# Kernel tuning notes

Measured on AMD Instinct MI355X. Metric: run time of the kernel, lower is better.

Reference implementation:

```python
import jax, jax.numpy as jnp
import numpy as np
import math

NUM_HEADS = 16
CONSTITUENCY_PENALTY = 0.5
CONSTITUENT_BLOCK = 64  # deterministic stand-in for the ChomskyParser constituency spans


def constituency_penalty_mask(seq_len, dtype):
    # Tokens in the same constituent (contiguous block) attend freely;
    # cross-constituent pairs are penalized by CONSTITUENCY_PENALTY.
    blk = jnp.arange(seq_len) // CONSTITUENT_BLOCK
    return jnp.where(blk[:, None] != blk[None, :], CONSTITUENCY_PENALTY, 0.0).astype(dtype)


def setup_inputs() -> dict:
    key = jax.random.key(0)
    ks = jax.random.split(key, 7)
    B, S, H = 8, 1024, 1024
    scale = 1.0 / math.sqrt(H)
    return {
        "hidden_states": jax.random.normal(ks[0], (B, S, H), jnp.float32),
        "Wq": jax.random.normal(ks[1], (H, H), jnp.float32) * scale,
        "bq": jnp.zeros((H,), jnp.float32),
        "Wk": jax.random.normal(ks[2], (H, H), jnp.float32) * scale,
        "bk": jnp.zeros((H,), jnp.float32),
        "Wv": jax.random.normal(ks[3], (H, H), jnp.float32) * scale,
        "bv": jnp.zeros((H,), jnp.float32),
    }


def reference(hidden_states, Wq, bq, Wk, bk, Wv, bv):
    B, S, H = hidden_states.shape
    nh = NUM_HEADS
    hd = H // nh

    def heads(x):  # [B,S,H] -> [B,nh,S,hd]
        return x.reshape(B, S, nh, hd).transpose(0, 2, 1, 3)

    q = heads(hidden_states @ Wq + bq)
    k = heads(hidden_states @ Wk + bk)
    v = heads(hidden_states @ Wv + bv)

    scores = jnp.einsum("bhqd,bhkd->bhqk", q, k) / jnp.sqrt(jnp.asarray(hd, q.dtype))
    # constituency penalty subtracted before softmax (broadcast over batch, heads)
    scores = scores - constituency_penalty_mask(S, scores.dtype)[None, None, :, :]
    probs = jax.nn.softmax(scores, axis=-1)  # dropout is identity in eval

    ctx = jnp.einsum("bhqk,bhkd->bhqd", probs, v)
    ctx = ctx.transpose(0, 2, 1, 3).reshape(B, S, H)
    return ctx
```

## Files before the change

kernel.cpp:

```cpp
#include <hip/hip_runtime.h>
#include <cstdint>

#define BB 8
#define SQ 1024
#define HH 1024
#define NH 16
#define HD 64

typedef __attribute__((ext_vector_type(4))) float f32x4;
typedef __attribute__((ext_vector_type(8))) __bf16 bf16x8;
typedef __attribute__((ext_vector_type(8))) unsigned short u16x8;
typedef __attribute__((ext_vector_type(4))) unsigned short u16x4;

__device__ __forceinline__ unsigned short f2bf(float f){
  uint32_t u = __builtin_bit_cast(uint32_t, f);
  u += 0x7FFFu + ((u >> 16) & 1u);
  return (unsigned short)(u >> 16);
}

__device__ __forceinline__ void gload_lds16(const void* g, void* l){
  __builtin_amdgcn_global_load_lds((__attribute__((address_space(1))) void*)g,
                                   (__attribute__((address_space(3))) void*)l,
                                   16, 0, 0);
}

__global__ __launch_bounds__(256) void k_prep(const float* __restrict__ x,
                                              unsigned short* __restrict__ xb,
                                              const float* __restrict__ Wq,
                                              const float* __restrict__ Wk,
                                              const float* __restrict__ Wv,
                                              unsigned short* __restrict__ wt){
  __shared__ float t[32][33];
  int bid = blockIdx.x, tid = threadIdx.x;
  if(bid < 4096){
    int i = bid * 256 + tid;
    const f32x4* xv = (const f32x4*)x;
    f32x4 a = xv[2*i], b = xv[2*i+1];
    u16x8 o;
    o[0]=f2bf(a[0]); o[1]=f2bf(a[1]); o[2]=f2bf(a[2]); o[3]=f2bf(a[3]);
    o[4]=f2bf(b[0]); o[5]=f2bf(b[1]); o[6]=f2bf(b[2]); o[7]=f2bf(b[3]);
    ((u16x8*)xb)[i] = o;
  } else {
    int idx = bid - 4096;
    int p = idx >> 10, rem = idx & 1023;
    const float* W = (p==0)?Wq:((p==1)?Wk:Wv);
    int n0 = (rem & 31)*32, k0 = (rem >> 5)*32;
    int tx = tid & 31, ty = tid >> 5;
    #pragma unroll
    for(int j=0;j<32;j+=8) t[ty+j][tx] = W[(size_t)(k0+ty+j)*HH + n0+tx];
    __syncthreads();
    unsigned short* o = wt + (size_t)p*HH*HH;
    #pragma unroll
    for(int j=0;j<32;j+=8) o[(size_t)(n0+ty+j)*HH + k0+tx] = f2bf(t[tx][ty+j]);
  }
}

#define BM 128
#define BN 128
#define BK 64
__global__ __launch_bounds__(256) void k_qkv(const unsigned short* __restrict__ Xb,
                                             const unsigned short* __restrict__ Wt,
                                             const float* __restrict__ bq,
                                             const float* __restrict__ bk,
                                             const float* __restrict__ bv,
                                             unsigned short* __restrict__ q_ws,
                                             unsigned short* __restrict__ k_ws,
                                             unsigned short* __restrict__ vt_ws){
  __shared__ __align__(16) unsigned short As[BM*BK];
  __shared__ __align__(16) unsigned short Bs[BN*BK];
  int tid = threadIdx.x;
  int lane = tid & 63, wid = tid >> 6;
  int nt = blockIdx.x % 24, mt = blockIdx.x / 24;
  int m0 = mt*BM, n0 = nt*BN;
  int wm = (wid & 1)*64, wn = (wid >> 1)*64;
  int lr = lane & 15, g = lane >> 4;

  const f32x4 zf = {0.f,0.f,0.f,0.f};
  f32x4 acc[4][4];
  #pragma unroll
  for(int a=0;a<4;a++)
    #pragma unroll
    for(int b=0;b<4;b++) acc[a][b] = zf;

  for(int kk=0; kk<1024; kk+=BK){
    __syncthreads();
    #pragma unroll
    for(int it=0; it<4; it++){
      int slot = it*256 + tid;
      int row = slot >> 3, ch = (slot & 7) ^ (row & 7);
      gload_lds16(Xb + (size_t)(m0+row)*1024 + kk + ch*8, &As[slot*8]);
    }
    #pragma unroll
    for(int it=0; it<4; it++){
      int slot = it*256 + tid;
      int row = slot >> 3, ch = (slot & 7) ^ (row & 7);
      gload_lds16(Wt + (size_t)(n0+row)*1024 + kk + ch*8, &Bs[slot*8]);
    }
    __syncthreads();

    #pragma unroll
    for(int ks=0; ks<2; ks++){
      bf16x8 af[4], bfr[4];
      #pragma unroll
      for(int mi=0;mi<4;mi++){
        int r = wm + mi*16 + lr;
        af[mi] = *(const bf16x8*)&As[r*64 + (((ks*4+g) ^ (r&7))<<3)];
      }
      #pragma unroll
      for(int ni=0;ni<4;ni++){
        int r = wn + ni*16 + lr;
        bfr[ni] = *(const bf16x8*)&Bs[r*64 + (((ks*4+g) ^ (r&7))<<3)];
      }
      #pragma unroll
      for(int mi=0;mi<4;mi++)
        #pragma unroll
        for(int ni=0;ni<4;ni++)
          acc[mi][ni] = __builtin_amdgcn_mfma_f32_16x16x32_bf16(af[mi], bfr[ni], acc[mi][ni], 0,0,0);
    }
  }

  int proj = n0 >> 10;
  const float* bias = (proj==0)?bq:((proj==1)?bk:bv);
  const float QSCALE = 0.18033688f;
  #pragma unroll
  for(int mi=0;mi<4;mi++){
    #pragma unroll
    for(int ni=0;ni<4;ni++){
      int ncol = n0 + wn + ni*16 + lr;
      int hcol = ncol & 1023;
      int h = hcol >> 6, d = hcol & 63;
      float bval = bias[hcol];
      if(proj == 0){
        #pragma unroll
        for(int i=0;i<4;i++){
          int m = m0 + wm + mi*16 + g*4 + i;
          int b = m >> 10, s = m & 1023;
          q_ws[((size_t)(b*NH + h)*SQ + s)*HD + d] = f2bf((acc[mi][ni][i] + bval)*QSCALE);
        }
      } else if(proj == 1){
        #pragma unroll
        for(int i=0;i<4;i++){
          int m = m0 + wm + mi*16 + g*4 + i;
          int b = m >> 10, s = m & 1023;
          k_ws[((size_t)(b*NH + h)*SQ + s)*HD + d] = f2bf(acc[mi][ni][i] + bval);
        }
      } else {
        int m = m0 + wm + mi*16 + g*4;
        int b = m >> 10, s = m & 1023;
        u16x4 pk;
        #pragma unroll
        for(int i=0;i<4;i++) pk[i] = f2bf(acc[mi][ni][i] + bval);
        *(u16x4*)&vt_ws[((size_t)(b*NH + h)*HD + d)*SQ + s] = pk;
      }
    }
  }
}

__global__ __launch_bounds__(512) void k_attn(const unsigned short* __restrict__ q_ws,
                                              const unsigned short* __restrict__ k_ws,
                                              const unsigned short* __restrict__ vt_ws,
                                              float* __restrict__ out){
  __shared__ __align__(16) unsigned short Ks[2][64*64];
  __shared__ __align__(16) unsigned short Vs[2][64*64];
  __shared__ __align__(16) unsigned short Ps[8][32*64];
  int tid = threadIdx.x, lane = tid & 63, wid = tid >> 6;
  int lr = lane & 15, g = lane >> 4;
  int bid = blockIdx.x;
  int swz = (bid & 7)*64 + (bid >> 3);
  int qb = swz & 3, bh = swz >> 2;
  int qw = qb*256 + wid*32;
  const unsigned short* qp = q_ws + (size_t)bh*SQ*HD;
  const unsigned short* kp = k_ws + (size_t)bh*SQ*HD;
  const unsigned short* vp = vt_ws + (size_t)bh*HD*SQ;

  bf16x8 qf[2][2];
  #pragma unroll
  for(int ns=0;ns<2;ns++)
    #pragma unroll
    for(int ks=0;ks<2;ks++)
      qf[ns][ks] = *(const bf16x8*)&qp[(size_t)(qw + ns*16 + lr)*HD + ks*32 + g*8];

  int diag = qw >> 6;

  int srow = tid >> 3;
  int sch  = (tid & 7) ^ (srow & 7);

  const f32x4 zf = {0.f,0.f,0.f,0.f};
  float lacc[2] = {0.f, 0.f};
  f32x4 co[4][2];
  #pragma unroll
  for(int ms=0;ms<4;ms++)
    #pragma unroll
    for(int ns=0;ns<2;ns++) co[ms][ns] = zf;

  unsigned short* Pw = &Ps[wid][0];

  gload_lds16(kp + (size_t)srow*HD + sch*8, &Ks[0][tid*8]);
  gload_lds16(vp + (size_t)srow*SQ + sch*8, &Vs[0][tid*8]);
  __syncthreads();

  int cur = 0;
  for(int kt=0; kt<16; kt++){
    if(kt < 15){
      int kb = (kt+1)*64;
      gload_lds16(kp + (size_t)(kb+srow)*HD + sch*8, &Ks[cur^1][tid*8]);
      gload_lds16(vp + (size_t)srow*SQ + kb + sch*8, &Vs[cur^1][tid*8]);
    }

    f32x4 sc[4][2];
    #pragma unroll
    for(int ms=0;ms<4;ms++){
      int r = ms*16 + lr;
      bf16x8 kf0 = *(const bf16x8*)&Ks[cur][r*64 + ((g ^ (r&7))<<3)];
      bf16x8 kf1 = *(const bf16x8*)&Ks[cur][r*64 + (((4+g) ^ (r&7))<<3)];
      #pragma unroll
      for(int ns=0;ns<2;ns++){
        sc[ms][ns] = __builtin_amdgcn_mfma_f32_16x16x32_bf16(kf0, qf[ns][0], zf, 0,0,0);
        sc[ms][ns] = __builtin_amdgcn_mfma_f32_16x16x32_bf16(kf1, qf[ns][1], sc[ms][ns], 0,0,0);
      }
    }

    float add = (kt == diag) ? 0.72134752f : 0.0f;

    #pragma unroll
    for(int ms=0;ms<4;ms++){
      #pragma unroll
      for(int ns=0;ns<2;ns++){
        u16x4 pk;
        #pragma unroll
        for(int i=0;i<4;i++){
          float pv = __builtin_amdgcn_exp2f(sc[ms][ns][i] + add);
          lacc[ns] += pv;
          pk[i] = f2bf(pv);
        }
        int q = ns*16 + lr;
        int c = ms*2 + (g>>1);
        *(u16x4*)&Pw[q*64 + ((c ^ (q&7))<<3) + (g&1)*4] = pk;
      }
    }

    bf16x8 pf[2][2];
    #pragma unroll
    for(int ns=0;ns<2;ns++){
      int q = ns*16 + lr;
      pf[ns][0] = *(const bf16x8*)&Pw[q*64 + ((g ^ (q&7))<<3)];
      pf[ns][1] = *(const bf16x8*)&Pw[q*64 + (((4+g) ^ (q&7))<<3)];
    }
    #pragma unroll
    for(int ms=0;ms<4;ms++){
      int vr = ms*16 + lr;
      bf16x8 vf0 = *(const bf16x8*)&Vs[cur][vr*64 + ((g ^ (vr&7))<<3)];
      bf16x8 vf1 = *(const bf16x8*)&Vs[cur][vr*64 + (((4+g) ^ (vr&7))<<3)];
      #pragma unroll
      for(int ns=0;ns<2;ns++){
        co[ms][ns] = __builtin_amdgcn_mfma_f32_16x16x32_bf16(vf0, pf[ns][0], co[ms][ns], 0,0,0);
        co[ms][ns] = __builtin_amdgcn_mfma_f32_16x16x32_bf16(vf1, pf[ns][1], co[ms][ns], 0,0,0);
      }
    }

    __syncthreads();
    cur ^= 1;
  }

  float rl[2];
  #pragma unroll
  for(int ns=0;ns<2;ns++){
    float l = lacc[ns];
    l += __shfl_xor(l, 16);
    l += __shfl_xor(l, 32);
    rl[ns] = 1.0f / l;
  }
  int b = bh >> 4, h = bh & 15;
  #pragma unroll
  for(int ms=0;ms<4;ms++){
    #pragma unroll
    for(int ns=0;ns<2;ns++){
      int q = qw + ns*16 + lr;
      int d = h*HD + ms*16 + g*4;
      f32x4 r = co[ms][ns];
      r[0]*=rl[ns]; r[1]*=rl[ns]; r[2]*=rl[ns]; r[3]*=rl[ns];
      *(f32x4*)&out[((size_t)(b*SQ + q))*HH + d] = r;
    }
  }
}

extern "C" void kernel_launch(void* const* d_in, const int* in_sizes, int n_in,
                              void* d_out, int out_size, void* d_ws, size_t ws_size,
                              hipStream_t stream){
  const float* hs = (const float*)d_in[0];
  const float* Wq = (const float*)d_in[1];
  const float* bq = (const float*)d_in[2];
  const float* Wk = (const float*)d_in[3];
  const float* bk = (const float*)d_in[4];
  const float* Wv = (const float*)d_in[5];
  const float* bv = (const float*)d_in[6];
  float* out = (float*)d_out;

  unsigned char* ws = (unsigned char*)d_ws;
  const size_t NX = (size_t)8192*1024;
  unsigned short* xb    = (unsigned short*)ws;
  unsigned short* wt    = (unsigned short*)(ws + NX*2);
  unsigned short* q_ws  = (unsigned short*)(ws + NX*2 + (size_t)3*1024*1024*2);
  unsigned short* k_ws  = q_ws + NX;
  unsigned short* vt_ws = k_ws + NX;

  k_prep<<<7168, 256, 0, stream>>>(hs, xb, Wq, Wk, Wv, wt);
  k_qkv<<<24*64, 256, 0, stream>>>(xb, wt, bq, bk, bv, q_ws, k_ws, vt_ws);
  k_attn<<<512, 512, 0, stream>>>(q_ws, k_ws, vt_ws, out);
}
```

Baseline: 223.6 us.

## Use 32x32x16 MFMA and register-resident P via permlane32 swap in attention

The attention kernel switches from 16x16x32 to 32x32x16 bf16 MFMA tiles, so each wave computes a 32-query by 32-key score block. The probabilities are repacked in registers with v_permlane32_swap instead of going through a per-wave LDS buffer, which removes the P shared-memory round trip and frees 32KB of LDS. Launch bounds now request 4 blocks per CU to raise occupancy. The cost is higher register pressure from 16-wide accumulators and dependence on the exact MFMA operand layout.

```diff
diff --git a/kernel.cpp b/kernel.cpp
--- a/kernel.cpp
+++ b/kernel.cpp
@@ -8,9 +8,11 @@
 #define HD 64
 
 typedef __attribute__((ext_vector_type(4))) float f32x4;
+typedef __attribute__((ext_vector_type(16))) float f32x16;
 typedef __attribute__((ext_vector_type(8))) __bf16 bf16x8;
 typedef __attribute__((ext_vector_type(8))) unsigned short u16x8;
 typedef __attribute__((ext_vector_type(4))) unsigned short u16x4;
+typedef __attribute__((ext_vector_type(4))) unsigned int u32x4;
 
 __device__ __forceinline__ unsigned short f2bf(float f){
   uint32_t u = __builtin_bit_cast(uint32_t, f);
@@ -156,15 +158,14 @@
   }
 }
 
-__global__ __launch_bounds__(512) void k_attn(const unsigned short* __restrict__ q_ws,
-                                              const unsigned short* __restrict__ k_ws,
-                                              const unsigned short* __restrict__ vt_ws,
-                                              float* __restrict__ out){
+__global__ __launch_bounds__(512, 4) void k_attn(const unsigned short* __restrict__ q_ws,
+                                                 const unsigned short* __restrict__ k_ws,
+                                                 const unsigned short* __restrict__ vt_ws,
+                                                 float* __restrict__ out){
   __shared__ __align__(16) unsigned short Ks[2][64*64];
   __shared__ __align__(16) unsigned short Vs[2][64*64];
-  __shared__ __align__(16) unsigned short Ps[8][32*64];
   int tid = threadIdx.x, lane = tid & 63, wid = tid >> 6;
-  int lr = lane & 15, g = lane >> 4;
+  int lq = lane & 31, h5 = lane >> 5;
   int bid = blockIdx.x;
   int swz = (bid & 7)*64 + (bid >> 3);
   int qb = swz & 3, bh = swz >> 2;
@@ -173,27 +174,22 @@
   const unsigned short* kp = k_ws + (size_t)bh*SQ*HD;
   const unsigned short* vp = vt_ws + (size_t)bh*HD*SQ;
 
-  bf16x8 qf[2][2];
-  #pragma unroll
-  for(int ns=0;ns<2;ns++)
-    #pragma unroll
-    for(int ks=0;ks<2;ks++)
-      qf[ns][ks] = *(const bf16x8*)&qp[(size_t)(qw + ns*16 + lr)*HD + ks*32 + g*8];
+  bf16x8 qf[4];
+  #pragma unroll
+  for(int dk=0;dk<4;dk++)
+    qf[dk] = *(const bf16x8*)&qp[(size_t)(qw + lq)*HD + dk*16 + h5*8];
 
   int diag = qw >> 6;
 
   int srow = tid >> 3;
   int sch  = (tid & 7) ^ (srow & 7);
 
-  const f32x4 zf = {0.f,0.f,0.f,0.f};
-  float lacc[2] = {0.f, 0.f};
-  f32x4 co[4][2];
-  #pragma unroll
-  for(int ms=0;ms<4;ms++)
-    #pragma unroll
-    for(int ns=0;ns<2;ns++) co[ms][ns] = zf;
-
-  unsigned short* Pw = &Ps[wid][0];
+  f32x16 co[2];
+  #pragma unroll
+  for(int db=0;db<2;db++)
+    #pragma unroll
+    for(int r=0;r<16;r++) co[db][r] = 0.f;
+  float lacc = 0.f;
 
   gload_lds16(kp + (size_t)srow*HD + sch*8, &Ks[0][tid*8]);
   gload_lds16(vp + (size_t)srow*SQ + sch*8, &Vs[0][tid*8]);
@@ -206,55 +202,43 @@
       gload_lds16(kp + (size_t)(kb+srow)*HD + sch*8, &Ks[cur^1][tid*8]);
       gload_lds16(vp + (size_t)srow*SQ + kb + sch*8, &Vs[cur^1][tid*8]);
     }
-
-    f32x4 sc[4][2];
-    #pragma unroll
-    for(int ms=0;ms<4;ms++){
-      int r = ms*16 + lr;
-      bf16x8 kf0 = *(const bf16x8*)&Ks[cur][r*64 + ((g ^ (r&7))<<3)];
-      bf16x8 kf1 = *(const bf16x8*)&Ks[cur][r*64 + (((4+g) ^ (r&7))<<3)];
-      #pragma unroll
-      for(int ns=0;ns<2;ns++){
-        sc[ms][ns] = __builtin_amdgcn_mfma_f32_16x16x32_bf16(kf0, qf[ns][0], zf, 0,0,0);
-        sc[ms][ns] = __builtin_amdgcn_mfma_f32_16x16x32_bf16(kf1, qf[ns][1], sc[ms][ns], 0,0,0);
-      }
-    }
-
     float add = (kt == diag) ? 0.72134752f : 0.0f;
 
     #pragma unroll
-    for(int ms=0;ms<4;ms++){
-      #pragma unroll
-      for(int ns=0;ns<2;ns++){
-        u16x4 pk;
-        #pragma unroll
-        for(int i=0;i<4;i++){
-          float pv = __builtin_amdgcn_exp2f(sc[ms][ns][i] + add);
-          lacc[ns] += pv;
-          pk[i] = f2bf(pv);
-        }
-        int q = ns*16 + lr;
-        int c = ms*2 + (g>>1);
-        *(u16x4*)&Pw[q*64 + ((c ^ (q&7))<<3) + (g&1)*4] = pk;
-      }
-    }
-
-    bf16x8 pf[2][2];
-    #pragma unroll
-    for(int ns=0;ns<2;ns++){
-      int q = ns*16 + lr;
-      pf[ns][0] = *(const bf16x8*)&Pw[q*64 + ((g ^ (q&7))<<3)];
-      pf[ns][1] = *(const bf16x8*)&Pw[q*64 + (((4+g) ^ (q&7))<<3)];
-    }
-    #pragma unroll
-    for(int ms=0;ms<4;ms++){
-      int vr = ms*16 + lr;
-      bf16x8 vf0 = *(const bf16x8*)&Vs[cur][vr*64 + ((g ^ (vr&7))<<3)];
-      bf16x8 vf1 = *(const bf16x8*)&Vs[cur][vr*64 + (((4+g) ^ (vr&7))<<3)];
-      #pragma unroll
-      for(int ns=0;ns<2;ns++){
-        co[ms][ns] = __builtin_amdgcn_mfma_f32_16x16x32_bf16(vf0, pf[ns][0], co[ms][ns], 0,0,0);
-        co[ms][ns] = __builtin_amdgcn_mfma_f32_16x16x32_bf16(vf1, pf[ns][1], co[ms][ns], 0,0,0);
+    for(int tb=0; tb<2; tb++){
+      f32x16 sc;
+      #pragma unroll
+      for(int r=0;r<16;r++) sc[r] = 0.f;
+      int r0 = tb*32 + lq;
+      #pragma unroll
+      for(int dk=0;dk<4;dk++){
+        bf16x8 kf = *(const bf16x8*)&Ks[cur][r0*64 + (((2*dk + h5) ^ (r0&7))<<3)];
+        sc = __builtin_amdgcn_mfma_f32_32x32x16_bf16(kf, qf[dk], sc, 0,0,0);
+      }
+      unsigned int pk[8];
+      #pragma unroll
+      for(int w=0;w<8;w++){
+        float lo = __builtin_amdgcn_exp2f(sc[2*w] + add);
+        float hi = __builtin_amdgcn_exp2f(sc[2*w+1] + add);
+        lacc += lo + hi;
+        pk[w] = (unsigned int)f2bf(lo) | ((unsigned int)f2bf(hi) << 16);
+      }
+      asm volatile("v_permlane32_swap_b32 %0, %1" : "+v"(pk[0]), "+v"(pk[2]));
+      asm volatile("v_permlane32_swap_b32 %0, %1" : "+v"(pk[1]), "+v"(pk[3]));
+      asm volatile("v_permlane32_swap_b32 %0, %1" : "+v"(pk[4]), "+v"(pk[6]));
+      asm volatile("v_permlane32_swap_b32 %0, %1" : "+v"(pk[5]), "+v"(pk[7]));
+      u32x4 w0 = {pk[0], pk[1], pk[2], pk[3]};
+      u32x4 w1 = {pk[4], pk[5], pk[6], pk[7]};
+      bf16x8 pf0 = __builtin_bit_cast(bf16x8, w0);
+      bf16x8 pf1 = __builtin_bit_cast(bf16x8, w1);
+
+      #pragma unroll
+      for(int db=0;db<2;db++){
+        int vr = db*32 + lq;
+        bf16x8 vf0 = *(const bf16x8*)&Vs[cur][vr*64 + (((4*tb + h5) ^ (vr&7))<<3)];
+        co[db] = __builtin_amdgcn_mfma_f32_32x32x16_bf16(vf0, pf0, co[db], 0,0,0);
+        bf16x8 vf1 = *(const bf16x8*)&Vs[cur][vr*64 + (((4*tb + 2 + h5) ^ (vr&7))<<3)];
+        co[db] = __builtin_amdgcn_mfma_f32_32x32x16_bf16(vf1, pf1, co[db], 0,0,0);
       }
     }
 
@@ -262,24 +246,21 @@
     cur ^= 1;
   }
 
-  float rl[2];
-  #pragma unroll
-  for(int ns=0;ns<2;ns++){
-    float l = lacc[ns];
-    l += __shfl_xor(l, 16);
-    l += __shfl_xor(l, 32);
-    rl[ns] = 1.0f / l;
-  }
+  lacc += __shfl_xor(lacc, 32);
+  float rl = 1.0f / lacc;
+
   int b = bh >> 4, h = bh & 15;
-  #pragma unroll
-  for(int ms=0;ms<4;ms++){
-    #pragma unroll
-    for(int ns=0;ns<2;ns++){
-      int q = qw + ns*16 + lr;
-      int d = h*HD + ms*16 + g*4;
-      f32x4 r = co[ms][ns];
-      r[0]*=rl[ns]; r[1]*=rl[ns]; r[2]*=rl[ns]; r[3]*=rl[ns];
-      *(f32x4*)&out[((size_t)(b*SQ + q))*HH + d] = r;
+  size_t obase = ((size_t)(b*SQ + qw + lq))*HH + h*HD;
+  #pragma unroll
+  for(int db=0;db<2;db++){
+    #pragma unroll
+    for(int w=0;w<4;w++){
+      f32x4 r;
+      r[0] = co[db][4*w  ] * rl;
+      r[1] = co[db][4*w+1] * rl;
+      r[2] = co[db][4*w+2] * rl;
+      r[3] = co[db][4*w+3] * rl;
+      *(f32x4*)&out[obase + db*32 + 8*w + 4*h5] = r;
     }
   }
 }
```

Result: faster. 219.1 us (-2.0%).
